# Kernel optimization log

Hardware: AMD Instinct MI355X
Metric: run time of the kernel (lower is better)

## Reference

```python
import jax, jax.numpy as jnp
import numpy as np

N_GROUPS = 32
EPS = 1e-5
N_HEADS = 8
D_K = 64


def setup_inputs() -> dict:
    key = jax.random.key(0)
    ks = jax.random.split(key, 4)
    B, C, H, W = 16, 512, 32, 32
    x = jax.random.normal(ks[0], (B, C, H, W), dtype=jnp.float32)
    gn_w = jnp.ones((C,), dtype=jnp.float32)
    gn_b = jnp.zeros((C,), dtype=jnp.float32)
    proj_w = jax.random.normal(ks[1], (3 * C, C), dtype=jnp.float32) * (C ** -0.5)
    proj_b = jnp.zeros((3 * C,), dtype=jnp.float32)
    out_w = jax.random.normal(ks[2], (C, C), dtype=jnp.float32) * (C ** -0.5)
    out_b = jnp.zeros((C,), dtype=jnp.float32)
    return {"x": x, "gn_w": gn_w, "gn_b": gn_b, "proj_w": proj_w,
            "proj_b": proj_b, "out_w": out_w, "out_b": out_b}


def _group_norm(x, w, b):
    B, C, H, W = x.shape
    xg = x.reshape(B, N_GROUPS, C // N_GROUPS, H, W)
    mean = xg.mean(axis=(2, 3, 4), keepdims=True)
    var = xg.var(axis=(2, 3, 4), keepdims=True)
    xn = (xg - mean) * jax.lax.rsqrt(var + EPS)
    xn = xn.reshape(B, C, H, W)
    return xn * w[None, :, None, None] + b[None, :, None, None]


def reference(x, gn_w, gn_b, proj_w, proj_b, out_w, out_b):
    B, C, H, W = x.shape
    S = H * W
    scale = D_K ** -0.25  # applied to both q and k, as in the original
    h = _group_norm(x, gn_w, gn_b).reshape(B, C, S).transpose(0, 2, 1)  # [B,S,C]
    qkv = h @ proj_w.T + proj_b  # [B,S,3C]
    qkv = qkv.reshape(B, S, N_HEADS, 3 * D_K)
    q, k, v = jnp.split(qkv, 3, axis=-1)  # each [B,S,H,D]
    attn = jnp.einsum('bihd,bjhd->bijh', q * scale, k * scale)  # [B,S,S,Hd]
    attn = jax.nn.softmax(attn, axis=2)
    res = jnp.einsum('bijh,bjhd->bihd', attn, v).reshape(B, S, N_HEADS * D_K)
    res = res @ out_w.T + out_b  # [B,S,C]
    res = res.transpose(0, 2, 1).reshape(B, C, H, W)
    return res + x
```

## Files before the change

kernel.cpp:

```cpp
#include <hip/hip_runtime.h>
#include <stdint.h>

typedef unsigned short u16;
typedef __attribute__((ext_vector_type(8))) short bf16x8;
typedef __attribute__((ext_vector_type(4))) short bf16x4;
typedef __attribute__((ext_vector_type(4))) float f32x4;
typedef __attribute__((ext_vector_type(4))) unsigned short u16x4;

#define GLD16(gp, lp) __builtin_amdgcn_global_load_lds( \
    (__attribute__((address_space(1))) void*)(void*)(gp), \
    (__attribute__((address_space(3))) void*)(void*)(lp), 16, 0, 0)

__device__ __forceinline__ u16 f2b(float f) {
  union { float f; unsigned u; } v; v.f = f;
  unsigned r = v.u + 0x7FFFu + ((v.u >> 16) & 1u);
  return (u16)(r >> 16);
}

__device__ __forceinline__ float fexp2(float x) {
#if __has_builtin(__builtin_amdgcn_exp2f)
  return __builtin_amdgcn_exp2f(x);
#else
  return exp2f(x);
#endif
}

__global__ __launch_bounds__(256) void cvt_kernel(const float* __restrict__ wq_f,
                                                  const float* __restrict__ wo_f,
                                                  u16* __restrict__ wq,
                                                  u16* __restrict__ wo) {
  int i = blockIdx.x * 256 + threadIdx.x;
  const float* src; u16* dst; int j;
  if (i < 196608) { src = wq_f; dst = wq; j = i; }
  else            { src = wo_f; dst = wo; j = i - 196608; }
  const float4 f = ((const float4*)src)[j];
  u16x4 r; r[0] = f2b(f.x); r[1] = f2b(f.y); r[2] = f2b(f.z); r[3] = f2b(f.w);
  *(u16x4*)(dst + (size_t)j * 4) = r;
}

__global__ __launch_bounds__(256) void gn_kernel(const float* __restrict__ x,
                                                 const float* __restrict__ gw,
                                                 const float* __restrict__ gb,
                                                 u16* __restrict__ h) {
  const int b = blockIdx.x >> 5, g = blockIdx.x & 31;
  const float* xg = x + ((size_t)(b * 512 + g * 16)) * 1024;
  const int tid = threadIdx.x;
  float vals[64];
  float s = 0.f, ss = 0.f;
#pragma unroll
  for (int i = 0; i < 64; i++) {
    float vv = xg[i * 256 + tid];
    vals[i] = vv; s += vv; ss += vv * vv;
  }
#pragma unroll
  for (int off = 32; off; off >>= 1) { s += __shfl_down(s, off); ss += __shfl_down(ss, off); }
  __shared__ float red[8];
  const int wid = tid >> 6, lane = tid & 63;
  if (lane == 0) { red[wid] = s; red[4 + wid] = ss; }
  __syncthreads();
  if (tid == 0) {
    float S = red[0] + red[1] + red[2] + red[3];
    float SS = red[4] + red[5] + red[6] + red[7];
    float mean = S * (1.f / 16384.f);
    float var = SS * (1.f / 16384.f) - mean * mean;
    red[0] = mean; red[1] = rsqrtf(var + 1e-5f);
  }
  __syncthreads();
  const float mean = red[0], rs = red[1];
  float sc[16], bi[16];
#pragma unroll
  for (int c = 0; c < 16; c++) { sc[c] = gw[g * 16 + c] * rs; bi[c] = gb[g * 16 + c]; }
#pragma unroll
  for (int h4 = 0; h4 < 4; h4++) {
    const int sp = h4 * 256 + tid;
    u16 row[16];
#pragma unroll
    for (int c = 0; c < 16; c++)
      row[c] = f2b((vals[c * 4 + h4] - mean) * sc[c] + bi[c]);
    u16* dst = h + ((size_t)(b * 1024 + sp)) * 512 + g * 16;
    *(bf16x8*)dst = *(bf16x8*)&row[0];
    *(bf16x8*)(dst + 8) = *(bf16x8*)&row[8];
  }
}

__global__ __launch_bounds__(256) void qkv_gemm(const u16* __restrict__ h,
                                                const u16* __restrict__ w,
                                                const float* __restrict__ bias,
                                                u16* __restrict__ q,
                                                u16* __restrict__ k,
                                                u16* __restrict__ v) {
  __shared__ u16 As[128 * 32];
  __shared__ u16 Bs[128 * 32];
  const int b = blockIdx.z;
  const int bm = blockIdx.x;
  const int bn = blockIdx.y;
  const int tid = threadIdx.x, lane = tid & 63, wid = tid >> 6;
  const int wm = wid & 1, wn = wid >> 1;
  const u16* gA = h + ((size_t)b * 1024 + bm * 128) * 512;
  const u16* gB = w + (size_t)bn * 128 * 512;

  const f32x4 fz = {0.f, 0.f, 0.f, 0.f};
  f32x4 acc[4][4];
#pragma unroll
  for (int i = 0; i < 4; i++)
#pragma unroll
    for (int j = 0; j < 4; j++) acc[i][j] = fz;

  const int r0 = lane >> 2;
  const int ch8 = (lane & 3) * 8;

  for (int kt = 0; kt < 16; ++kt) {
    __syncthreads();
#pragma unroll
    for (int j = 0; j < 2; ++j) {
      const int idx = wid * 2 + j;
      const int row = idx * 16 + r0;
      GLD16(gA + (size_t)row * 512 + kt * 32 + ch8, &As[idx * 512 + lane * 8]);
      GLD16(gB + (size_t)row * 512 + kt * 32 + ch8, &Bs[idx * 512 + lane * 8]);
    }
    __syncthreads();
    bf16x8 af[4], bf[4];
#pragma unroll
    for (int mi = 0; mi < 4; mi++)
      af[mi] = *(const bf16x8*)&As[(wm * 64 + mi * 16 + (lane & 15)) * 32 + (lane >> 4) * 8];
#pragma unroll
    for (int ni = 0; ni < 4; ni++)
      bf[ni] = *(const bf16x8*)&Bs[(wn * 64 + ni * 16 + (lane & 15)) * 32 + (lane >> 4) * 8];
#pragma unroll
    for (int mi = 0; mi < 4; mi++)
#pragma unroll
      for (int ni = 0; ni < 4; ni++)
        acc[mi][ni] = __builtin_amdgcn_mfma_f32_16x16x32_bf16(af[mi], bf[ni], acc[mi][ni], 0, 0, 0);
  }

  const float qscale = 0.51006972f;
  const float kscale = 0.35355339059327373f;
  const int quad4 = (lane >> 4) << 2;
#pragma unroll
  for (int mi = 0; mi < 4; mi++) {
    const int m = bm * 128 + wm * 64 + mi * 16 + quad4;
#pragma unroll
    for (int ni = 0; ni < 4; ni++) {
      const int n = bn * 128 + wn * 64 + ni * 16 + (lane & 15);
      const int head = n / 192;
      const int rr = n - head * 192;
      const float bi = bias[n];
      const int d = rr & 63;
      if (rr < 128) {
        u16* dst = (rr < 64) ? q : k;
        const float sc = (rr < 64) ? qscale : kscale;
        dst += ((size_t)(b * 8 + head) * 1024 + m) * 64 + d;
#pragma unroll
        for (int r = 0; r < 4; r++)
          dst[(size_t)r * 64] = f2b((acc[mi][ni][r] + bi) * sc);
      } else {
        u16x4 pk;
#pragma unroll
        for (int r = 0; r < 4; r++) pk[r] = f2b(acc[mi][ni][r] + bi);
        *(u16x4*)(v + ((size_t)(b * 8 + head) * 64 + d) * 1024 + m) = pk;
      }
    }
  }
}

__global__ __launch_bounds__(256) void attn_kernel(const u16* __restrict__ q,
                                                   const u16* __restrict__ k,
                                                   const u16* __restrict__ vT,
                                                   u16* __restrict__ o) {
  __shared__ u16 Ks[2][64 * 64];
  __shared__ u16 Vs[2][64 * 64];
  const int bh = blockIdx.x;
  const int qb = blockIdx.y;
  const int tid = threadIdx.x, lane = tid & 63, wid = tid >> 6;
  const u16* Q = q + (size_t)bh * 1024 * 64;
  const u16* K = k + (size_t)bh * 1024 * 64;
  const u16* V = vT + (size_t)bh * 64 * 1024;
  const int qrow0 = qb * 128 + wid * 32;
  const int c15 = lane & 15, quad = lane >> 4;
  const int sw = c15 & 7;
  const int srow = tid >> 2;
  const int t4 = tid & 3;
  const int s7 = srow & 7;
  const int kld0 = srow * 64 + (((t4 * 2) ^ s7) * 8);
  const int kld1 = srow * 64 + (((t4 * 2 + 1) ^ s7) * 8);
  int vld[4];
#pragma unroll
  for (int qq = 0; qq < 4; qq++)
    vld[qq] = srow * 64 + ((((t4 >> 1) * 4 + qq) ^ s7) * 8) + (t4 & 1) * 4;

  bf16x8 qf[2][2];
#pragma unroll
  for (int kk = 0; kk < 2; kk++)
#pragma unroll
    for (int ni = 0; ni < 2; ni++)
      qf[kk][ni] = *(const bf16x8*)(Q + (size_t)(qrow0 + ni * 16 + c15) * 64 + kk * 32 + quad * 8);

  const f32x4 fz = {0.f, 0.f, 0.f, 0.f};
  const float Mshift = 14.4269504089f;
  const f32x4 fm = {-Mshift, -Mshift, -Mshift, -Mshift};
  f32x4 oaccT[4][2];
#pragma unroll
  for (int i = 0; i < 4; i++)
#pragma unroll
    for (int j = 0; j < 2; j++) oaccT[i][j] = fz;
  float lsum[2] = {0.f, 0.f};

  bf16x8 kr0, kr1, vr0, vr1;
  {
    const u16* Kn = K + (size_t)srow * 64 + t4 * 16;
    kr0 = *(const bf16x8*)(Kn); kr1 = *(const bf16x8*)(Kn + 8);
    const u16* Vn = V + (size_t)srow * 1024 + t4 * 16;
    vr0 = *(const bf16x8*)(Vn); vr1 = *(const bf16x8*)(Vn + 8);
  }
  {
    u16* Kd = Ks[0]; u16* Vd = Vs[0];
    *(bf16x8*)&Kd[kld0] = kr0; *(bf16x8*)&Kd[kld1] = kr1;
    union { bf16x4 h[2]; bf16x8 v; } a0, a1;
    a0.v = vr0; a1.v = vr1;
    *(bf16x4*)&Vd[vld[0]] = a0.h[0];
    *(bf16x4*)&Vd[vld[1]] = a0.h[1];
    *(bf16x4*)&Vd[vld[2]] = a1.h[0];
    *(bf16x4*)&Vd[vld[3]] = a1.h[1];
  }
  {
    const u16* Kn = K + (size_t)(64 + srow) * 64 + t4 * 16;
    kr0 = *(const bf16x8*)(Kn); kr1 = *(const bf16x8*)(Kn + 8);
    const u16* Vn = V + (size_t)srow * 1024 + 64 + t4 * 16;
    vr0 = *(const bf16x8*)(Vn); vr1 = *(const bf16x8*)(Vn + 8);
  }

  for (int kt = 0; kt < 16; ++kt) {
    __syncthreads();
    const int cur = kt & 1, alt = cur ^ 1;
    if (kt < 15) {
      u16* Kd = Ks[alt]; u16* Vd = Vs[alt];
      *(bf16x8*)&Kd[kld0] = kr0; *(bf16x8*)&Kd[kld1] = kr1;
      union { bf16x4 h[2]; bf16x8 v; } a0, a1;
      a0.v = vr0; a1.v = vr1;
      *(bf16x4*)&Vd[vld[0]] = a0.h[0];
      *(bf16x4*)&Vd[vld[1]] = a0.h[1];
      *(bf16x4*)&Vd[vld[2]] = a1.h[0];
      *(bf16x4*)&Vd[vld[3]] = a1.h[1];
      const int pk2 = (kt + 2) & 15;
      const u16* Kn = K + ((size_t)pk2 * 64 + srow) * 64 + t4 * 16;
      kr0 = *(const bf16x8*)(Kn); kr1 = *(const bf16x8*)(Kn + 8);
      const u16* Vn = V + (size_t)srow * 1024 + pk2 * 64 + t4 * 16;
      vr0 = *(const bf16x8*)(Vn); vr1 = *(const bf16x8*)(Vn + 8);
    }
    const u16* Kc = Ks[cur];
    const u16* Vc = Vs[cur];

    f32x4 sacc[4][2];
#pragma unroll
    for (int i = 0; i < 4; i++)
#pragma unroll
      for (int j = 0; j < 2; j++) sacc[i][j] = fm;
#pragma unroll
    for (int kk = 0; kk < 2; kk++) {
      bf16x8 af[4];
#pragma unroll
      for (int mi = 0; mi < 4; mi++)
        af[mi] = *(const bf16x8*)&Kc[(mi * 16 + c15) * 64 + (((kk * 4 + quad) ^ sw) * 8)];
#pragma unroll
      for (int mi = 0; mi < 4; mi++)
#pragma unroll
        for (int ni = 0; ni < 2; ni++)
          sacc[mi][ni] = __builtin_amdgcn_mfma_f32_16x16x32_bf16(af[mi], qf[kk][ni], sacc[mi][ni], 0, 0, 0);
    }

    unsigned pkd[4][2][2];
#pragma unroll
    for (int ni = 0; ni < 2; ni++) {
      float ls = 0.f;
#pragma unroll
      for (int mi = 0; mi < 4; mi++) {
        unsigned pu[4];
#pragma unroll
        for (int r = 0; r < 4; r++) {
          const float p = fexp2(sacc[mi][ni][r]);
          ls += p;
          union { float f; unsigned u; } c; c.f = p;
          pu[r] = c.u;
        }
        pkd[mi][ni][0] = __builtin_amdgcn_perm(pu[1], pu[0], 0x07060302u);
        pkd[mi][ni][1] = __builtin_amdgcn_perm(pu[3], pu[2], 0x07060302u);
      }
      lsum[ni] += ls;
    }

#pragma unroll
    for (int mg = 0; mg < 2; mg++) {
      union { unsigned u[4]; bf16x8 v; } bb[2];
#pragma unroll
      for (int ni = 0; ni < 2; ni++) {
        bb[ni].u[0] = pkd[2 * mg][ni][0];     bb[ni].u[1] = pkd[2 * mg][ni][1];
        bb[ni].u[2] = pkd[2 * mg + 1][ni][0]; bb[ni].u[3] = pkd[2 * mg + 1][ni][1];
      }
#pragma unroll
      for (int nd = 0; nd < 4; nd++) {
        const bf16x8 aa = *(const bf16x8*)&Vc[(nd * 16 + c15) * 64 + (((mg * 4 + quad) ^ sw) * 8)];
#pragma unroll
        for (int ni = 0; ni < 2; ni++)
          oaccT[nd][ni] = __builtin_amdgcn_mfma_f32_16x16x32_bf16(aa, bb[ni].v, oaccT[nd][ni], 0, 0, 0);
      }
    }
  }

  float iv[2];
#pragma unroll
  for (int ni = 0; ni < 2; ni++) {
    float l = lsum[ni];
    l += __shfl_xor(l, 16);
    l += __shfl_xor(l, 32);
    iv[ni] = 1.f / l;
  }
  const int b = bh >> 3, hh = bh & 7;
#pragma unroll
  for (int ni = 0; ni < 2; ni++) {
    const int row = qrow0 + ni * 16 + c15;
#pragma unroll
    for (int nd = 0; nd < 4; nd++) {
      u16x4 pk4;
#pragma unroll
      for (int r = 0; r < 4; r++) pk4[r] = f2b(oaccT[nd][ni][r] * iv[ni]);
      *(u16x4*)(o + ((size_t)b * 1024 + row) * 512 + hh * 64 + nd * 16 + quad * 4) = pk4;
    }
  }
}

__global__ __launch_bounds__(256) void out_gemm(const u16* __restrict__ wo,
                                                const u16* __restrict__ attn,
                                                const float* __restrict__ ob,
                                                const float* __restrict__ x,
                                                float* __restrict__ out) {
  __shared__ u16 As[128 * 32];
  __shared__ u16 Bs[128 * 32];
  const int b = blockIdx.z;
  const int bm = blockIdx.x;
  const int bn = blockIdx.y;
  const int tid = threadIdx.x, lane = tid & 63, wid = tid >> 6;
  const int wm = wid & 1, wn = wid >> 1;
  const u16* gA = wo + (size_t)bm * 128 * 512;
  const u16* gB = attn + ((size_t)b * 1024 + bn * 128) * 512;

  const f32x4 fz = {0.f, 0.f, 0.f, 0.f};
  f32x4 acc[4][4];
#pragma unroll
  for (int i = 0; i < 4; i++)
#pragma unroll
    for (int j = 0; j < 4; j++) acc[i][j] = fz;

  const int r0 = lane >> 2;
  const int ch8 = (lane & 3) * 8;

  for (int kt = 0; kt < 16; ++kt) {
    __syncthreads();
#pragma unroll
    for (int j = 0; j < 2; ++j) {
      const int idx = wid * 2 + j;
      const int row = idx * 16 + r0;
      GLD16(gA + (size_t)row * 512 + kt * 32 + ch8, &As[idx * 512 + lane * 8]);
      GLD16(gB + (size_t)row * 512 + kt * 32 + ch8, &Bs[idx * 512 + lane * 8]);
    }
    __syncthreads();
    bf16x8 af[4], bf[4];
#pragma unroll
    for (int mi = 0; mi < 4; mi++)
      af[mi] = *(const bf16x8*)&As[(wm * 64 + mi * 16 + (lane & 15)) * 32 + (lane >> 4) * 8];
#pragma unroll
    for (int ni = 0; ni < 4; ni++)
      bf[ni] = *(const bf16x8*)&Bs[(wn * 64 + ni * 16 + (lane & 15)) * 32 + (lane >> 4) * 8];
#pragma unroll
    for (int mi = 0; mi < 4; mi++)
#pragma unroll
      for (int ni = 0; ni < 4; ni++)
        acc[mi][ni] = __builtin_amdgcn_mfma_f32_16x16x32_bf16(af[mi], bf[ni], acc[mi][ni], 0, 0, 0);
  }

  const int quad4 = (lane >> 4) << 2;
#pragma unroll
  for (int mi = 0; mi < 4; mi++) {
    const int c = bm * 128 + wm * 64 + mi * 16 + quad4;
#pragma unroll
    for (int ni = 0; ni < 4; ni++) {
      const int s = bn * 128 + wn * 64 + ni * 16 + (lane & 15);
#pragma unroll
      for (int r = 0; r < 4; r++) {
        const int cc = c + r;
        const size_t idx = ((size_t)b * 512 + cc) * 1024 + s;
        out[idx] = acc[mi][ni][r] + ob[cc] + x[idx];
      }
    }
  }
}

extern "C" void kernel_launch(void* const* d_in, const int* in_sizes, int n_in,
                              void* d_out, int out_size, void* d_ws, size_t ws_size,
                              hipStream_t stream) {
  const float* x      = (const float*)d_in[0];
  const float* gn_w   = (const float*)d_in[1];
  const float* gn_b   = (const float*)d_in[2];
  const float* proj_w = (const float*)d_in[3];
  const float* proj_b = (const float*)d_in[4];
  const float* out_w  = (const float*)d_in[5];
  const float* out_b  = (const float*)d_in[6];
  float* out = (float*)d_out;

  char* p = (char*)d_ws;
  u16* h    = (u16*)p; p += (size_t)16 * 1024 * 512 * 2;
  u16* q    = (u16*)p; p += (size_t)16 * 8 * 1024 * 64 * 2;
  u16* k    = (u16*)p; p += (size_t)16 * 8 * 1024 * 64 * 2;
  u16* v    = (u16*)p; p += (size_t)16 * 8 * 1024 * 64 * 2;
  u16* attn = (u16*)p; p += (size_t)16 * 1024 * 512 * 2;
  u16* wq   = (u16*)p; p += (size_t)1536 * 512 * 2;
  u16* wo   = (u16*)p; p += (size_t)512 * 512 * 2;

  cvt_kernel<<<1024, 256, 0, stream>>>(proj_w, out_w, wq, wo);
  gn_kernel<<<512, 256, 0, stream>>>(x, gn_w, gn_b, h);
  qkv_gemm<<<dim3(8, 12, 16), 256, 0, stream>>>(h, wq, proj_b, q, k, v);
  attn_kernel<<<dim3(128, 8, 1), 256, 0, stream>>>(q, k, v, attn);
  out_gemm<<<dim3(4, 8, 16), 256, 0, stream>>>(wo, attn, out_b, x, out);
}
```

Before: 218.3 us.

## Use 512-thread attention blocks with 256 query rows and MFMA priority hints

```diff
diff --git a/kernel.cpp b/kernel.cpp
--- a/kernel.cpp
+++ b/kernel.cpp
@@ -163,7 +163,7 @@
   }
 }
 
-__global__ __launch_bounds__(256) void attn_kernel(const u16* __restrict__ q,
+__global__ __launch_bounds__(512) void attn_kernel(const u16* __restrict__ q,
                                                    const u16* __restrict__ k,
                                                    const u16* __restrict__ vT,
                                                    u16* __restrict__ o) {
@@ -175,18 +175,17 @@
   const u16* Q = q + (size_t)bh * 1024 * 64;
   const u16* K = k + (size_t)bh * 1024 * 64;
   const u16* V = vT + (size_t)bh * 64 * 1024;
-  const int qrow0 = qb * 128 + wid * 32;
+  const int qrow0 = qb * 256 + wid * 32;
   const int c15 = lane & 15, quad = lane >> 4;
   const int sw = c15 & 7;
-  const int srow = tid >> 2;
-  const int t4 = tid & 3;
+  const int srow = tid >> 3;
+  const int u8g  = tid & 7;
   const int s7 = srow & 7;
-  const int kld0 = srow * 64 + (((t4 * 2) ^ s7) * 8);
-  const int kld1 = srow * 64 + (((t4 * 2 + 1) ^ s7) * 8);
-  int vld[4];
-#pragma unroll
-  for (int qq = 0; qq < 4; qq++)
-    vld[qq] = srow * 64 + ((((t4 >> 1) * 4 + qq) ^ s7) * 8) + (t4 & 1) * 4;
+  const int kld = srow * 64 + ((u8g ^ s7) * 8);
+  const int ve = 4 * (u8g >> 2) + 2 * (u8g & 1);
+  const int vc = ((u8g >> 1) & 1) * 4;
+  const int vld0 = srow * 64 + ((ve ^ s7) * 8) + vc;
+  const int vld1 = srow * 64 + (((ve + 1) ^ s7) * 8) + vc;
 
   bf16x8 qf[2][2];
 #pragma unroll
@@ -205,47 +204,31 @@
     for (int j = 0; j < 2; j++) oaccT[i][j] = fz;
   float lsum[2] = {0.f, 0.f};
 
-  bf16x8 kr0, kr1, vr0, vr1;
-  {
-    const u16* Kn = K + (size_t)srow * 64 + t4 * 16;
-    kr0 = *(const bf16x8*)(Kn); kr1 = *(const bf16x8*)(Kn + 8);
-    const u16* Vn = V + (size_t)srow * 1024 + t4 * 16;
-    vr0 = *(const bf16x8*)(Vn); vr1 = *(const bf16x8*)(Vn + 8);
-  }
+  bf16x8 kr, vr;
+  kr = *(const bf16x8*)(K + (size_t)srow * 64 + u8g * 8);
+  vr = *(const bf16x8*)(V + (size_t)srow * 1024 + u8g * 8);
   {
     u16* Kd = Ks[0]; u16* Vd = Vs[0];
-    *(bf16x8*)&Kd[kld0] = kr0; *(bf16x8*)&Kd[kld1] = kr1;
-    union { bf16x4 h[2]; bf16x8 v; } a0, a1;
-    a0.v = vr0; a1.v = vr1;
-    *(bf16x4*)&Vd[vld[0]] = a0.h[0];
-    *(bf16x4*)&Vd[vld[1]] = a0.h[1];
-    *(bf16x4*)&Vd[vld[2]] = a1.h[0];
-    *(bf16x4*)&Vd[vld[3]] = a1.h[1];
-  }
-  {
-    const u16* Kn = K + (size_t)(64 + srow) * 64 + t4 * 16;
-    kr0 = *(const bf16x8*)(Kn); kr1 = *(const bf16x8*)(Kn + 8);
-    const u16* Vn = V + (size_t)srow * 1024 + 64 + t4 * 16;
-    vr0 = *(const bf16x8*)(Vn); vr1 = *(const bf16x8*)(Vn + 8);
-  }
+    *(bf16x8*)&Kd[kld] = kr;
+    union { bf16x4 h[2]; bf16x8 v; } a; a.v = vr;
+    *(bf16x4*)&Vd[vld0] = a.h[0];
+    *(bf16x4*)&Vd[vld1] = a.h[1];
+  }
+  kr = *(const bf16x8*)(K + (size_t)(64 + srow) * 64 + u8g * 8);
+  vr = *(const bf16x8*)(V + (size_t)srow * 1024 + 64 + u8g * 8);
 
   for (int kt = 0; kt < 16; ++kt) {
     __syncthreads();
     const int cur = kt & 1, alt = cur ^ 1;
     if (kt < 15) {
       u16* Kd = Ks[alt]; u16* Vd = Vs[alt];
-      *(bf16x8*)&Kd[kld0] = kr0; *(bf16x8*)&Kd[kld1] = kr1;
-      union { bf16x4 h[2]; bf16x8 v; } a0, a1;
-      a0.v = vr0; a1.v = vr1;
-      *(bf16x4*)&Vd[vld[0]] = a0.h[0];
-      *(bf16x4*)&Vd[vld[1]] = a0.h[1];
-      *(bf16x4*)&Vd[vld[2]] = a1.h[0];
-      *(bf16x4*)&Vd[vld[3]] = a1.h[1];
+      *(bf16x8*)&Kd[kld] = kr;
+      union { bf16x4 h[2]; bf16x8 v; } a; a.v = vr;
+      *(bf16x4*)&Vd[vld0] = a.h[0];
+      *(bf16x4*)&Vd[vld1] = a.h[1];
       const int pk2 = (kt + 2) & 15;
-      const u16* Kn = K + ((size_t)pk2 * 64 + srow) * 64 + t4 * 16;
-      kr0 = *(const bf16x8*)(Kn); kr1 = *(const bf16x8*)(Kn + 8);
-      const u16* Vn = V + (size_t)srow * 1024 + pk2 * 64 + t4 * 16;
-      vr0 = *(const bf16x8*)(Vn); vr1 = *(const bf16x8*)(Vn + 8);
+      kr = *(const bf16x8*)(K + ((size_t)pk2 * 64 + srow) * 64 + u8g * 8);
+      vr = *(const bf16x8*)(V + (size_t)srow * 1024 + pk2 * 64 + u8g * 8);
     }
     const u16* Kc = Ks[cur];
     const u16* Vc = Vs[cur];
@@ -261,11 +244,13 @@
 #pragma unroll
       for (int mi = 0; mi < 4; mi++)
         af[mi] = *(const bf16x8*)&Kc[(mi * 16 + c15) * 64 + (((kk * 4 + quad) ^ sw) * 8)];
+      __builtin_amdgcn_s_setprio(1);
 #pragma unroll
       for (int mi = 0; mi < 4; mi++)
 #pragma unroll
         for (int ni = 0; ni < 2; ni++)
           sacc[mi][ni] = __builtin_amdgcn_mfma_f32_16x16x32_bf16(af[mi], qf[kk][ni], sacc[mi][ni], 0, 0, 0);
+      __builtin_amdgcn_s_setprio(0);
     }
 
     unsigned pkd[4][2][2];
@@ -296,13 +281,17 @@
         bb[ni].u[0] = pkd[2 * mg][ni][0];     bb[ni].u[1] = pkd[2 * mg][ni][1];
         bb[ni].u[2] = pkd[2 * mg + 1][ni][0]; bb[ni].u[3] = pkd[2 * mg + 1][ni][1];
       }
-#pragma unroll
-      for (int nd = 0; nd < 4; nd++) {
-        const bf16x8 aa = *(const bf16x8*)&Vc[(nd * 16 + c15) * 64 + (((mg * 4 + quad) ^ sw) * 8)];
+      bf16x8 aa[4];
+#pragma unroll
+      for (int nd = 0; nd < 4; nd++)
+        aa[nd] = *(const bf16x8*)&Vc[(nd * 16 + c15) * 64 + (((mg * 4 + quad) ^ sw) * 8)];
+      __builtin_amdgcn_s_setprio(1);
+#pragma unroll
+      for (int nd = 0; nd < 4; nd++)
 #pragma unroll
         for (int ni = 0; ni < 2; ni++)
-          oaccT[nd][ni] = __builtin_amdgcn_mfma_f32_16x16x32_bf16(aa, bb[ni].v, oaccT[nd][ni], 0, 0, 0);
-      }
+          oaccT[nd][ni] = __builtin_amdgcn_mfma_f32_16x16x32_bf16(aa[nd], bb[ni].v, oaccT[nd][ni], 0, 0, 0);
+      __builtin_amdgcn_s_setprio(0);
     }
   }
 
@@ -418,6 +407,6 @@
   cvt_kernel<<<1024, 256, 0, stream>>>(proj_w, out_w, wq, wo);
   gn_kernel<<<512, 256, 0, stream>>>(x, gn_w, gn_b, h);
   qkv_gemm<<<dim3(8, 12, 16), 256, 0, stream>>>(h, wq, proj_b, q, k, v);
-  attn_kernel<<<dim3(128, 8, 1), 256, 0, stream>>>(q, k, v, attn);
+  attn_kernel<<<dim3(128, 4), 512, 0, stream>>>(q, k, v, attn);
   out_gemm<<<dim3(4, 8, 16), 256, 0, stream>>>(wo, attn, out_b, x, out);
 }
```

Result: faster. 207.9 us (-4.8%).
